# Kernel optimization log

Measured on AMD Instinct MI355X. Metric: run time of the kernel, lower is better.

Reference implementation:

```python
import jax, jax.numpy as jnp
import numpy as np

B, D, N, NKV, H = 8, 256, 2048, 2048, 4
DH = D // H
EPS = 1e-5


def _pw(W, b, t):
    # pointwise Conv1d (kernel_size=1): [out,in] x [B,in,N] -> [B,out,N]
    return jnp.einsum('oi,bin->bon', W, t) + b[None, :, None]


def setup_inputs() -> dict:
    key = jax.random.key(0)
    ks = jax.random.split(key, 16)
    s = 0.05
    inp = {
        'x': jax.random.normal(ks[0], (B, D, N), jnp.float32),
        'source': jax.random.normal(ks[1], (B, D, NKV), jnp.float32),
        'mask': jax.random.uniform(ks[2], (B, N, NKV), jnp.float32),
        'Wq': jax.random.normal(ks[3], (D, D), jnp.float32) * s,
        'bq': jax.random.normal(ks[4], (D,), jnp.float32) * s,
        'Wk': jax.random.normal(ks[5], (D, D), jnp.float32) * s,
        'bk': jax.random.normal(ks[6], (D,), jnp.float32) * s,
        'Wv': jax.random.normal(ks[7], (D, D), jnp.float32) * s,
        'bv': jax.random.normal(ks[8], (D,), jnp.float32) * s,
        'Wm': jax.random.normal(ks[9], (D, D), jnp.float32) * s,
        'bm': jax.random.normal(ks[10], (D,), jnp.float32) * s,
        'W1': jax.random.normal(ks[11], (2 * D, 2 * D), jnp.float32) * s,
        'b1': jax.random.normal(ks[12], (2 * D,), jnp.float32) * s,
        'W2': jax.random.normal(ks[13], (D, 2 * D), jnp.float32) * s,
        'b2': jnp.zeros((D,), jnp.float32),  # nn.init.constant_(mlp[-1].bias, 0)
    }
    return inp


def reference(x, source, mask, Wq, bq, Wk, bk, Wv, bv, Wm, bm, W1, b1, W2, b2):
    b = x.shape[0]
    # projections, then split channels D -> (dh, H) as torch .view does
    q = _pw(Wq, bq, x).reshape(b, DH, H, -1)       # [B,dh,H,N]
    k = _pw(Wk, bk, source).reshape(b, DH, H, -1)  # [B,dh,H,M]
    v = _pw(Wv, bv, source).reshape(b, DH, H, -1)  # [B,dh,H,M]
    scores = jnp.einsum('bdhn,bdhm->bhnm', q, k) / jnp.sqrt(jnp.float32(DH))
    scores = scores * mask[:, None, :, :]          # multiplicative mask
    prob = jax.nn.softmax(scores, axis=-1)
    attn = jnp.einsum('bhnm,bdhm->bdhn', prob, v).reshape(b, D, -1)
    message = _pw(Wm, bm, attn)                    # merge conv
    y = jnp.concatenate([x, message], axis=1)      # [B,2D,N]
    y = _pw(W1, b1, y)
    # InstanceNorm1d (affine=False): normalize over N per (batch, channel)
    mu = jnp.mean(y, axis=-1, keepdims=True)
    var = jnp.var(y, axis=-1, keepdims=True)
    y = jax.nn.relu((y - mu) / jnp.sqrt(var + EPS))
    return _pw(W2, b2, y)
```

## Files before the change

### kernel.cpp

```cpp
#include <hip/hip_runtime.h>
#include <hip/hip_bf16.h>
#include <math.h>

#define B_  8
#define D_  256
#define N_  2048
#define M_  2048
#define H_  4

typedef __attribute__((ext_vector_type(8))) short bf16x8;
typedef __attribute__((ext_vector_type(4))) float f32x4;

static __device__ __forceinline__ unsigned short f2bf(float f) {
    __hip_bfloat16 h = __float2bfloat16(f);
    return *reinterpret_cast<unsigned short*>(&h);
}
static __device__ __forceinline__ float bf2f_lo(unsigned int u) {
    return __uint_as_float((u & 0xffffu) << 16);
}
static __device__ __forceinline__ float bf2f_hi(unsigned int u) {
    return __uint_as_float(u & 0xffff0000u);
}

#define GLOAD16(gsrc, ldsbase)                                                     \
    __builtin_amdgcn_global_load_lds(                                              \
        (const __attribute__((address_space(1))) unsigned int*)(gsrc),             \
        (__attribute__((address_space(3))) unsigned int*)(ldsbase), 16, 0, 0)

__global__ __launch_bounds__(256) void cvt_w(
    const float* __restrict__ Wq, const float* __restrict__ Wk,
    const float* __restrict__ Wv, const float* __restrict__ Wm,
    const float* __restrict__ W1, const float* __restrict__ W2,
    const float* __restrict__ bq, const float* __restrict__ bk,
    unsigned short* __restrict__ wqp, unsigned short* __restrict__ wkp,
    unsigned short* __restrict__ wv,  unsigned short* __restrict__ wmp,
    unsigned short* __restrict__ w1b, unsigned short* __restrict__ w2b,
    float* __restrict__ bqp, float* __restrict__ bkp)
{
    const int idx = blockIdx.x * 256 + threadIdx.x;
    if (idx < 65536) {
        const int op = idx >> 8, k = idx & 255;
        const int h = op >> 6, dh = op & 63;
        wqp[idx] = f2bf(Wq[(dh*4 + h)*256 + k]);
    } else if (idx < 131072) {
        const int j = idx - 65536;
        const int op = j >> 8, k = j & 255;
        const int h = op >> 6, dh = op & 63;
        wkp[j] = f2bf(Wk[(dh*4 + h)*256 + k]);
    } else if (idx < 196608) {
        const int j = idx - 131072;
        wv[j] = f2bf(Wv[j]);
    } else if (idx < 262144) {
        const int j = idx - 196608;
        const int o = j >> 8, cp = j & 255;
        const int h = cp >> 6, dh = cp & 63;
        wmp[j] = f2bf(Wm[o*256 + dh*4 + h]);
    } else if (idx < 524288) {
        const int j = idx - 262144;
        w1b[j] = f2bf(W1[j]);
    } else if (idx < 655360) {
        const int j = idx - 524288;
        w2b[j] = f2bf(W2[j]);
    } else if (idx < 655616) {
        const int j = idx - 655360;
        const int h = j >> 6, dh = j & 63;
        bqp[j] = bq[dh*4 + h];
    } else {
        const int j = idx - 655616;
        const int h = j >> 6, dh = j & 63;
        bkp[j] = bk[dh*4 + h];
    }
}

__global__ __launch_bounds__(256) void cvt_t(
    const float* __restrict__ x, const float* __restrict__ src,
    unsigned short* __restrict__ xbf, unsigned short* __restrict__ sbf)
{
    __shared__ float T[64][65];
    const int z = blockIdx.z;
    const int b = z & 7;
    const float* in = (z < 8) ? x : src;
    unsigned short* out = (z < 8) ? xbf : sbf;
    const int c0 = blockIdx.y * 64, n0 = blockIdx.x * 64;
    const int tid = threadIdx.x;
    #pragma unroll
    for (int u = 0; u < 16; ++u) {
        const int idx = u * 256 + tid;
        const int nn = idx & 63, cc = idx >> 6;
        T[cc][nn] = in[((size_t)(b*256 + c0 + cc))*2048 + n0 + nn];
    }
    __syncthreads();
    #pragma unroll
    for (int u = 0; u < 16; ++u) {
        const int idx = u * 256 + tid;
        const int c = idx & 63, nn = idx >> 6;
        out[((size_t)(b*2048 + n0 + nn))*256 + c0 + c] = f2bf(T[c][nn]);
    }
}

template<int CIN, int EPI>
__global__ __launch_bounds__(256, 2) void conv_mfma(
    const unsigned short* __restrict__ Wb, const float* __restrict__ bias,
    const unsigned short* __restrict__ inA, const unsigned short* __restrict__ inB,
    int splitC, void* __restrict__ outp)
{
    __shared__ __align__(16) unsigned short SH[32768];
    const int b  = blockIdx.z;
    const int o0 = blockIdx.y * 128;
    const int n0 = blockIdx.x * 128;
    const int tid = threadIdx.x;
    const int w = tid >> 6, l = tid & 63;
    const int wr = w >> 1, wc = w & 1;
    const int g_ = l >> 4, ln = l & 15;

    f32x4 acc[4][4];
    #pragma unroll
    for (int mi = 0; mi < 4; ++mi)
        #pragma unroll
        for (int nj = 0; nj < 4; ++nj) acc[mi][nj] = (f32x4){0.f, 0.f, 0.f, 0.f};

    auto STAGE = [&](int t, int c) {
        const int k0 = t * 64;
        unsigned short* As = SH + c * 16384;
        unsigned short* Bs = As + 8192;
        #pragma unroll
        for (int u = 0; u < 4; ++u) {
            const int chunk = (w*4 + u)*64 + l;
            const int row = chunk >> 3;
            const int cs = (chunk & 7) ^ (row & 7);
            const unsigned short* gp = Wb + (size_t)(o0 + row)*CIN + k0 + cs*8;
            GLOAD16(gp, As + (w*4 + u)*512);
        }
        const unsigned short* src; int sC, kk;
        if (k0 < splitC) { src = inA; sC = splitC; kk = k0; }
        else             { src = inB; sC = CIN - splitC; kk = k0 - splitC; }
        #pragma unroll
        for (int u = 0; u < 4; ++u) {
            const int chunk = (w*4 + u)*64 + l;
            const int row = chunk >> 3;
            const int cs = (chunk & 7) ^ (row & 7);
            const unsigned short* gp = src + ((size_t)b*N_ + n0 + row)*sC + kk + cs*8;
            GLOAD16(gp, Bs + (w*4 + u)*512);
        }
    };

    auto COMPUTE = [&](int c) {
        const unsigned short* As = SH + c * 16384;
        const unsigned short* Bs = As + 8192;
        #pragma unroll
        for (int ks = 0; ks < 2; ++ks) {
            bf16x8 af[4], bfr[4];
            #pragma unroll
            for (int mi = 0; mi < 4; ++mi) {
                const int row = wr*64 + mi*16 + ln;
                af[mi] = *(const bf16x8*)&As[row*64 + (((ks*4 + g_) ^ (row & 7)) << 3)];
            }
            #pragma unroll
            for (int nj = 0; nj < 4; ++nj) {
                const int row = wc*64 + nj*16 + ln;
                bfr[nj] = *(const bf16x8*)&Bs[row*64 + (((ks*4 + g_) ^ (row & 7)) << 3)];
            }
            #pragma unroll
            for (int mi = 0; mi < 4; ++mi)
                #pragma unroll
                for (int nj = 0; nj < 4; ++nj)
                    acc[mi][nj] = __builtin_amdgcn_mfma_f32_16x16x32_bf16(af[mi], bfr[nj], acc[mi][nj], 0, 0, 0);
        }
    };

    const int nt = CIN / 64;
    STAGE(0, 0);
    __syncthreads();
    int cur = 0;
    for (int t = 0; t < nt; ++t) {
        if (t + 1 < nt) STAGE(t + 1, cur ^ 1);
        COMPUTE(cur);
        __syncthreads();
        cur ^= 1;
    }

    if constexpr (EPI == 0 || EPI == 2) {
        unsigned short* Os = SH;
        #pragma unroll
        for (int mi = 0; mi < 4; ++mi) {
            const int ob = wr*64 + mi*16 + g_*4;
            const float4 bv = *(const float4*)&bias[o0 + ob];
            #pragma unroll
            for (int nj = 0; nj < 4; ++nj) {
                const int nl = wc*64 + nj*16 + ln;
                ushort4 us;
                us.x = f2bf(acc[mi][nj][0] + bv.x);
                us.y = f2bf(acc[mi][nj][1] + bv.y);
                us.z = f2bf(acc[mi][nj][2] + bv.z);
                us.w = f2bf(acc[mi][nj][3] + bv.w);
                *(ushort4*)&Os[nl*128 + (((ob >> 3) ^ (nl & 7)) << 3) + (ob & 4)] = us;
            }
        }
        __syncthreads();
        if constexpr (EPI == 0) {
            unsigned short* outT = (unsigned short*)outp;
            #pragma unroll
            for (int u = 0; u < 8; ++u) {
                const int idx = u*256 + tid;
                const int oc = idx & 15, n = idx >> 4;
                const uint4 v = *(const uint4*)&Os[n*128 + ((oc ^ (n & 7)) << 3)];
                const int og = o0 + oc*8;
                *(uint4*)&outT[(((size_t)b*H_ + (og >> 6))*N_ + n0 + n)*64 + (og & 63)] = v;
            }
        } else {
            unsigned short* outS = (unsigned short*)outp;
            const int ostride = gridDim.y * 128;
            #pragma unroll
            for (int u = 0; u < 8; ++u) {
                const int idx = u*256 + tid;
                const int oc = idx & 15, n = idx >> 4;
                const uint4 v = *(const uint4*)&Os[n*128 + ((oc ^ (n & 7)) << 3)];
                *(uint4*)&outS[((size_t)b*N_ + n0 + n)*ostride + o0 + oc*8] = v;
            }
        }
    } else if constexpr (EPI == 1) {
        unsigned short* Os = SH;
        #pragma unroll
        for (int mi = 0; mi < 4; ++mi) {
            const int ob = wr*64 + mi*16 + g_*4;
            const float4 bv = *(const float4*)&bias[o0 + ob];
            const float bb[4] = {bv.x, bv.y, bv.z, bv.w};
            #pragma unroll
            for (int nj = 0; nj < 4; ++nj) {
                const int nl = wc*64 + nj*16 + ln;
                #pragma unroll
                for (int r = 0; r < 4; ++r)
                    Os[(ob + r)*136 + nl] = f2bf(acc[mi][nj][r] + bb[r]);
            }
        }
        __syncthreads();
        unsigned short* outV = (unsigned short*)outp;
        #pragma unroll
        for (int u = 0; u < 8; ++u) {
            const int idx = u*256 + tid;
            const int mc = idx & 15, o = idx >> 4;
            const uint4 v = *(const uint4*)&Os[o*136 + mc*8];
            *(uint4*)&outV[((size_t)b*D_ + o0 + o)*(size_t)M_ + n0 + mc*8] = v;
        }
    } else {
        float* Of = (float*)SH;
        #pragma unroll
        for (int mi = 0; mi < 4; ++mi) {
            const int ob = wr*64 + mi*16 + g_*4;
            const float4 bv = *(const float4*)&bias[o0 + ob];
            const float bb[4] = {bv.x, bv.y, bv.z, bv.w};
            #pragma unroll
            for (int nj = 0; nj < 4; ++nj) {
                const int nl = wc*64 + nj*16 + ln;
                #pragma unroll
                for (int r = 0; r < 4; ++r) {
                    const int o_ = ob + r;
                    Of[o_*128 + ((((nl >> 2) ^ (o_ & 7)) << 2)) + (nl & 3)] = acc[mi][nj][r] + bb[r];
                }
            }
        }
        __syncthreads();
        float* outF = (float*)outp;
        #pragma unroll
        for (int u = 0; u < 16; ++u) {
            const int idx = u*256 + tid;
            const int nc = idx & 31, o = idx >> 5;
            const float4 v = *(const float4*)&Of[o*128 + ((nc ^ (o & 7)) << 2)];
            *(float4*)&outF[((size_t)b*D_ + o0 + o)*(size_t)N_ + n0 + nc*4] = v;
        }
    }
}

__global__ __launch_bounds__(256) void attn_mfma(
    const unsigned short* __restrict__ qt, const unsigned short* __restrict__ kt,
    const unsigned short* __restrict__ vbf, const float* __restrict__ mask,
    unsigned short* __restrict__ ab)
{
    __shared__ __align__(16) unsigned short SH[4 * 64 * 64];
    unsigned short* Qs = SH;
    unsigned short* Ks = SH + 4096;
    unsigned short* Vs = SH + 8192;
    unsigned short* Ps = SH + 12288;

    const int b = blockIdx.z, h = blockIdx.y, n0 = blockIdx.x * 64;
    const int tid = threadIdx.x;
    const int w = tid >> 6, lane = tid & 63;
    const int ln = lane & 15, g = lane >> 4;
    const int rsw = (ln & 7) << 3;

    #pragma unroll
    for (int u = 0; u < 4; ++u) {
        const int idx = u * 256 + tid;
        const int ch = idx & 15, n = idx >> 4;
        const ushort4 v = *(const ushort4*)&qt[(((size_t)b * H_ + h) * N_ + n0 + n) * 64 + ch*4];
        *(ushort4*)&Qs[n * 64 + ((ch*4) ^ ((n & 7) << 3))] = v;
    }

    f32x4 oacc[4];
    #pragma unroll
    for (int f = 0; f < 4; ++f) oacc[f] = (f32x4){0.f, 0.f, 0.f, 0.f};
    float mrun[4] = {-INFINITY, -INFINITY, -INFINITY, -INFINITY};
    float lrun[4] = {0.f, 0.f, 0.f, 0.f};

    __syncthreads();

    bf16x8 a_q[2];
    #pragma unroll
    for (int ks = 0; ks < 2; ++ks)
        a_q[ks] = *(const bf16x8*)&Qs[(w*16 + ln) * 64 + ((ks*32 + g*8) ^ rsw)];

    for (int m0 = 0; m0 < M_; m0 += 64) {
        #pragma unroll
        for (int u = 0; u < 4; ++u) {
            const int idx = u * 256 + tid;
            const int ch = idx & 15, r = idx >> 4;
            const ushort4 kv = *(const ushort4*)&kt[(((size_t)b * H_ + h) * M_ + m0 + r) * 64 + ch*4];
            *(ushort4*)&Ks[r * 64 + ((ch*4) ^ ((r & 7) << 3))] = kv;
            const ushort4 vv = *(const ushort4*)&vbf[((size_t)b * D_ + r * H_ + h) * M_ + m0 + ch*4];
            *(ushort4*)&Vs[r * 64 + ((ch*4) ^ ((r & 7) << 3))] = vv;
        }
        __syncthreads();

        float mk[4][4];
        #pragma unroll
        for (int r = 0; r < 4; ++r)
            #pragma unroll
            for (int f = 0; f < 4; ++f)
                mk[r][f] = mask[((size_t)b * N_ + n0 + w*16 + g*4 + r) * (size_t)M_ + m0 + f*16 + ln];

        f32x4 sacc[4];
        #pragma unroll
        for (int f = 0; f < 4; ++f) sacc[f] = (f32x4){0.f, 0.f, 0.f, 0.f};
        #pragma unroll
        for (int ks = 0; ks < 2; ++ks)
            #pragma unroll
            for (int f = 0; f < 4; ++f) {
                const bf16x8 bk = *(const bf16x8*)&Ks[(f*16 + ln) * 64 + ((ks*32 + g*8) ^ rsw)];
                sacc[f] = __builtin_amdgcn_mfma_f32_16x16x32_bf16(a_q[ks], bk, sacc[f], 0, 0, 0);
            }

        #pragma unroll
        for (int r = 0; r < 4; ++r) {
            float s0 = sacc[0][r] * 0.125f * mk[r][0];
            float s1 = sacc[1][r] * 0.125f * mk[r][1];
            float s2 = sacc[2][r] * 0.125f * mk[r][2];
            float s3 = sacc[3][r] * 0.125f * mk[r][3];
            float tmax = fmaxf(fmaxf(s0, s1), fmaxf(s2, s3));
            tmax = fmaxf(tmax, __shfl_xor(tmax, 1, 16));
            tmax = fmaxf(tmax, __shfl_xor(tmax, 2, 16));
            tmax = fmaxf(tmax, __shfl_xor(tmax, 4, 16));
            tmax = fmaxf(tmax, __shfl_xor(tmax, 8, 16));
            const float nm = fmaxf(mrun[r], tmax);
            const float corr = __expf(mrun[r] - nm);
            const float p0 = __expf(s0 - nm);
            const float p1 = __expf(s1 - nm);
            const float p2 = __expf(s2 - nm);
            const float p3 = __expf(s3 - nm);
            float ps = p0 + p1 + p2 + p3;
            ps += __shfl_xor(ps, 1, 16);
            ps += __shfl_xor(ps, 2, 16);
            ps += __shfl_xor(ps, 4, 16);
            ps += __shfl_xor(ps, 8, 16);
            lrun[r] = lrun[r] * corr + ps;
            mrun[r] = nm;
            #pragma unroll
            for (int f = 0; f < 4; ++f) oacc[f][r] *= corr;
            const int row = w*16 + g*4 + r;
            const int rs2 = (row & 7) << 3;
            Ps[row * 64 + ((0*16 + ln) ^ rs2)] = f2bf(p0);
            Ps[row * 64 + ((1*16 + ln) ^ rs2)] = f2bf(p1);
            Ps[row * 64 + ((2*16 + ln) ^ rs2)] = f2bf(p2);
            Ps[row * 64 + ((3*16 + ln) ^ rs2)] = f2bf(p3);
        }
        __syncthreads();

        #pragma unroll
        for (int ks = 0; ks < 2; ++ks) {
            const bf16x8 ap = *(const bf16x8*)&Ps[(w*16 + ln) * 64 + ((ks*32 + g*8) ^ rsw)];
            #pragma unroll
            for (int fd = 0; fd < 4; ++fd) {
                const bf16x8 bv = *(const bf16x8*)&Vs[(fd*16 + ln) * 64 + ((ks*32 + g*8) ^ rsw)];
                oacc[fd] = __builtin_amdgcn_mfma_f32_16x16x32_bf16(ap, bv, oacc[fd], 0, 0, 0);
            }
        }
        __syncthreads();
    }

    unsigned short* Os = SH;
    float inv[4];
    #pragma unroll
    for (int r = 0; r < 4; ++r) inv[r] = 1.f / lrun[r];
    #pragma unroll
    for (int fd = 0; fd < 4; ++fd) {
        const int dh = fd*16 + ln;
        const int cd = dh >> 3;
        #pragma unroll
        for (int r = 0; r < 4; ++r) {
            const int n = w*16 + g*4 + r;
            Os[n*64 + ((cd ^ (n & 7)) << 3) + (dh & 7)] = f2bf(oacc[fd][r] * inv[r]);
        }
    }
    __syncthreads();
    #pragma unroll
    for (int u = 0; u < 2; ++u) {
        const int idx = u*256 + tid;
        const int ch = idx & 7, n = idx >> 3;
        const uint4 v = *(const uint4*)&Os[n*64 + ((ch ^ (n & 7)) << 3)];
        *(uint4*)&ab[((size_t)b*N_ + n0 + n)*256 + h*64 + ch*8] = v;
    }
}

__global__ __launch_bounds__(256) void in_stats(
    const unsigned short* __restrict__ y1, float* __restrict__ st)
{
    const int b = blockIdx.y, nch = blockIdx.x, tid = threadIdx.x;
    const int c = tid * 2;
    float sa = 0.f, sa2 = 0.f, sb = 0.f, sb2 = 0.f;
    for (int r = 0; r < 128; ++r) {
        const int n = nch*128 + r;
        const unsigned int u = *(const unsigned int*)&y1[((size_t)b*N_ + n)*512 + c];
        const float a = bf2f_lo(u), bb = bf2f_hi(u);
        sa += a; sa2 += a*a; sb += bb; sb2 += bb*bb;
    }
    atomicAdd(&st[(b*512 + c)*2 + 0], sa);
    atomicAdd(&st[(b*512 + c)*2 + 1], sa2);
    atomicAdd(&st[(b*512 + c + 1)*2 + 0], sb);
    atomicAdd(&st[(b*512 + c + 1)*2 + 1], sb2);
}

__global__ __launch_bounds__(256) void in_apply(
    const unsigned short* __restrict__ y1, const float* __restrict__ st,
    unsigned short* __restrict__ yo)
{
    const int b = blockIdx.y, nch = blockIdx.x, tid = threadIdx.x;
    const int c = tid * 2;
    const float mua = st[(b*512 + c)*2 + 0] * (1.f/2048.f);
    const float vara = st[(b*512 + c)*2 + 1] * (1.f/2048.f) - mua*mua;
    const float inva = rsqrtf(vara + 1e-5f);
    const float mub = st[(b*512 + c + 1)*2 + 0] * (1.f/2048.f);
    const float varb = st[(b*512 + c + 1)*2 + 1] * (1.f/2048.f) - mub*mub;
    const float invb = rsqrtf(varb + 1e-5f);
    for (int r = 0; r < 128; ++r) {
        const int n = nch*128 + r;
        const size_t off = ((size_t)b*N_ + n)*512 + c;
        const unsigned int u = *(const unsigned int*)&y1[off];
        const float na = fmaxf((bf2f_lo(u) - mua) * inva, 0.f);
        const float nb = fmaxf((bf2f_hi(u) - mub) * invb, 0.f);
        const unsigned int pv = (unsigned int)f2bf(na) | ((unsigned int)f2bf(nb) << 16);
        *(unsigned int*)&yo[off] = pv;
    }
}

extern "C" void kernel_launch(void* const* d_in, const int* in_sizes, int n_in,
                              void* d_out, int out_size, void* d_ws, size_t ws_size,
                              hipStream_t stream)
{
    const float* x    = (const float*)d_in[0];
    const float* srcp = (const float*)d_in[1];
    const float* mask = (const float*)d_in[2];
    const float* Wq = (const float*)d_in[3];
    const float* bq = (const float*)d_in[4];
    const float* Wk = (const float*)d_in[5];
    const float* bk = (const float*)d_in[6];
    const float* Wv = (const float*)d_in[7];
    const float* bv = (const float*)d_in[8];
    const float* Wm = (const float*)d_in[9];
    const float* bm = (const float*)d_in[10];
    const float* W1 = (const float*)d_in[11];
    const float* b1 = (const float*)d_in[12];
    const float* W2 = (const float*)d_in[13];
    const float* b2 = (const float*)d_in[14];
    float* out = (float*)d_out;

    char* wsb = (char*)d_ws;
    const size_t MB = 1 << 20;
    unsigned short* xbf   = (unsigned short*)(wsb + 0*MB);
    unsigned short* srcbf = (unsigned short*)(wsb + 8*MB);
    unsigned short* ab    = (unsigned short*)(wsb + 8*MB);
    unsigned short* qt_   = (unsigned short*)(wsb + 16*MB);
    unsigned short* msg   = (unsigned short*)(wsb + 16*MB);
    unsigned short* kt_   = (unsigned short*)(wsb + 24*MB);
    unsigned short* y1    = (unsigned short*)(wsb + 24*MB);
    unsigned short* vb_   = (unsigned short*)(wsb + 32*MB);
    unsigned short* ybf   = (unsigned short*)(wsb + 40*MB);
    char* wbase = wsb + 56*MB;
    unsigned short* wqp = (unsigned short*)(wbase + 0);
    unsigned short* wkp = (unsigned short*)(wbase + 128*1024);
    unsigned short* wv  = (unsigned short*)(wbase + 256*1024);
    unsigned short* wmp = (unsigned short*)(wbase + 384*1024);
    unsigned short* w1b = (unsigned short*)(wbase + 512*1024);
    unsigned short* w2b = (unsigned short*)(wbase + 1024*1024);
    float* bqp   = (float*)(wbase + 1280*1024);
    float* bkp   = (float*)(wbase + 1281*1024);
    float* stats = (float*)(wbase + 1282*1024);

    const dim3 blk(256);

    cvt_w<<<dim3(2562), blk, 0, stream>>>(Wq, Wk, Wv, Wm, W1, W2, bq, bk,
                                          wqp, wkp, wv, wmp, w1b, w2b, bqp, bkp);
    cvt_t<<<dim3(32, 4, 16), blk, 0, stream>>>(x, srcp, xbf, srcbf);
    hipMemsetAsync(stats, 0, 8*512*2*sizeof(float), stream);

    conv_mfma<256, 0><<<dim3(16, 2, 8), blk, 0, stream>>>(wqp, bqp, xbf,   xbf, 256, qt_);
    conv_mfma<256, 0><<<dim3(16, 2, 8), blk, 0, stream>>>(wkp, bkp, srcbf, srcbf, 256, kt_);
    conv_mfma<256, 1><<<dim3(16, 2, 8), blk, 0, stream>>>(wv,  bv,  srcbf, srcbf, 256, vb_);

    attn_mfma<<<dim3(32, 4, 8), blk, 0, stream>>>(qt_, kt_, vb_, mask, ab);

    conv_mfma<256, 2><<<dim3(16, 2, 8), blk, 0, stream>>>(wmp, bm, ab, ab, 256, msg);
    conv_mfma<512, 2><<<dim3(16, 4, 8), blk, 0, stream>>>(w1b, b1, xbf, msg, 256, y1);

    in_stats<<<dim3(16, 8), blk, 0, stream>>>(y1, stats);
    in_apply<<<dim3(16, 8), blk, 0, stream>>>(y1, stats, ybf);

    conv_mfma<512, 4><<<dim3(16, 2, 8), blk, 0, stream>>>(w2b, b2, ybf, ybf, 512, out);
}
```

Before: 445.6 us.

## Fold merge conv into W1, fuse QKV convs, pipeline attention loads

Folds the merge projection (Wm, bm) algebraically into the second half of W1, which removes one full conv pass and its intermediate buffer. The three Q/K/V projections become a single launch. Conv tiles shrink to 64 columns so more blocks run, with higher occupancy bounds. Attention is rewritten to double-buffer K/V with async global-to-LDS loads, prefetch mask values, and use a different softmax update structure. The folded weight is rounded to bf16 after the product, which changes numerics slightly, and the instance-norm kernels get more blocks.

```diff
diff --git a/kernel.cpp b/kernel.cpp
--- a/kernel.cpp
+++ b/kernel.cpp
@@ -29,13 +29,14 @@
 
 __global__ __launch_bounds__(256) void cvt_w(
     const float* __restrict__ Wq, const float* __restrict__ Wk,
-    const float* __restrict__ Wv, const float* __restrict__ Wm,
-    const float* __restrict__ W1, const float* __restrict__ W2,
-    const float* __restrict__ bq, const float* __restrict__ bk,
+    const float* __restrict__ Wv, const float* __restrict__ W1,
+    const float* __restrict__ W2, const float* __restrict__ bq,
+    const float* __restrict__ bk, const float* __restrict__ b1,
+    const float* __restrict__ bm,
     unsigned short* __restrict__ wqp, unsigned short* __restrict__ wkp,
-    unsigned short* __restrict__ wv,  unsigned short* __restrict__ wmp,
-    unsigned short* __restrict__ w1b, unsigned short* __restrict__ w2b,
-    float* __restrict__ bqp, float* __restrict__ bkp)
+    unsigned short* __restrict__ wv,  unsigned short* __restrict__ wcat,
+    unsigned short* __restrict__ w2b,
+    float* __restrict__ bqp, float* __restrict__ bkp, float* __restrict__ bfold)
 {
     const int idx = blockIdx.x * 256 + threadIdx.x;
     if (idx < 65536) {
@@ -50,26 +51,72 @@
     } else if (idx < 196608) {
         const int j = idx - 131072;
         wv[j] = f2bf(Wv[j]);
-    } else if (idx < 262144) {
+    } else if (idx < 327680) {
         const int j = idx - 196608;
-        const int o = j >> 8, cp = j & 255;
-        const int h = cp >> 6, dh = cp & 63;
-        wmp[j] = f2bf(Wm[o*256 + dh*4 + h]);
-    } else if (idx < 524288) {
-        const int j = idx - 262144;
-        w1b[j] = f2bf(W1[j]);
-    } else if (idx < 655360) {
-        const int j = idx - 524288;
+        const int o = j >> 8, k = j & 255;
+        wcat[o*512 + k] = f2bf(W1[o*512 + k]);
+    } else if (idx < 458752) {
+        const int j = idx - 327680;
         w2b[j] = f2bf(W2[j]);
-    } else if (idx < 655616) {
-        const int j = idx - 655360;
+    } else if (idx < 459008) {
+        const int j = idx - 458752;
         const int h = j >> 6, dh = j & 63;
         bqp[j] = bq[dh*4 + h];
-    } else {
-        const int j = idx - 655616;
+    } else if (idx < 459264) {
+        const int j = idx - 459008;
         const int h = j >> 6, dh = j & 63;
         bkp[j] = bk[dh*4 + h];
-    }
+    } else if (idx < 459776) {
+        const int o = idx - 459264;
+        float acc = b1[o];
+        for (int j = 0; j < 256; ++j) acc += W1[o*512 + 256 + j] * bm[j];
+        bfold[o] = acc;
+    }
+}
+
+__global__ __launch_bounds__(256) void fold_w(
+    const float* __restrict__ W1, const float* __restrict__ Wm,
+    unsigned short* __restrict__ wcat)
+{
+    __shared__ float As[64][33];
+    __shared__ float Bs[32][64];
+    const int o0 = blockIdx.y * 64, c0 = blockIdx.x * 64;
+    const int tid = threadIdx.x;
+    const int tx = tid & 15, ty = tid >> 4;
+    float acc[4][4] = {};
+    for (int k0 = 0; k0 < 256; k0 += 32) {
+        #pragma unroll
+        for (int u = 0; u < 8; ++u) {
+            const int l = u * 256 + tid;
+            As[l >> 5][l & 31] = W1[(o0 + (l >> 5))*512 + 256 + k0 + (l & 31)];
+        }
+        #pragma unroll
+        for (int u = 0; u < 8; ++u) {
+            const int l = u * 256 + tid;
+            const int cp = c0 + (l & 63), j = k0 + (l >> 6);
+            const int h = cp >> 6, dh = cp & 63;
+            Bs[l >> 6][l & 63] = Wm[j*256 + dh*4 + h];
+        }
+        __syncthreads();
+        #pragma unroll 8
+        for (int kk = 0; kk < 32; ++kk) {
+            const float a0 = As[ty*4+0][kk];
+            const float a1 = As[ty*4+1][kk];
+            const float a2 = As[ty*4+2][kk];
+            const float a3 = As[ty*4+3][kk];
+            const float4 bv = *(const float4*)&Bs[kk][tx*4];
+            acc[0][0]+=a0*bv.x; acc[0][1]+=a0*bv.y; acc[0][2]+=a0*bv.z; acc[0][3]+=a0*bv.w;
+            acc[1][0]+=a1*bv.x; acc[1][1]+=a1*bv.y; acc[1][2]+=a1*bv.z; acc[1][3]+=a1*bv.w;
+            acc[2][0]+=a2*bv.x; acc[2][1]+=a2*bv.y; acc[2][2]+=a2*bv.z; acc[2][3]+=a2*bv.w;
+            acc[3][0]+=a3*bv.x; acc[3][1]+=a3*bv.y; acc[3][2]+=a3*bv.z; acc[3][3]+=a3*bv.w;
+        }
+        __syncthreads();
+    }
+    #pragma unroll
+    for (int i = 0; i < 4; ++i)
+        #pragma unroll
+        for (int j = 0; j < 4; ++j)
+            wcat[(o0 + ty*4 + i)*512 + 256 + c0 + tx*4 + j] = f2bf(acc[i][j]);
 }
 
 __global__ __launch_bounds__(256) void cvt_t(
@@ -99,71 +146,69 @@
 }
 
 template<int CIN, int EPI>
-__global__ __launch_bounds__(256, 2) void conv_mfma(
+static __device__ __forceinline__ void conv_body(
+    unsigned short* SH,
     const unsigned short* __restrict__ Wb, const float* __restrict__ bias,
     const unsigned short* __restrict__ inA, const unsigned short* __restrict__ inB,
-    int splitC, void* __restrict__ outp)
-{
-    __shared__ __align__(16) unsigned short SH[32768];
-    const int b  = blockIdx.z;
+    int splitC, void* __restrict__ outp, int ostride)
+{
+    const int b  = blockIdx.z & 7;
     const int o0 = blockIdx.y * 128;
-    const int n0 = blockIdx.x * 128;
+    const int n0 = blockIdx.x * 64;
     const int tid = threadIdx.x;
     const int w = tid >> 6, l = tid & 63;
     const int wr = w >> 1, wc = w & 1;
     const int g_ = l >> 4, ln = l & 15;
 
-    f32x4 acc[4][4];
+    f32x4 acc[4][2];
     #pragma unroll
     for (int mi = 0; mi < 4; ++mi)
         #pragma unroll
-        for (int nj = 0; nj < 4; ++nj) acc[mi][nj] = (f32x4){0.f, 0.f, 0.f, 0.f};
+        for (int nj = 0; nj < 2; ++nj) acc[mi][nj] = (f32x4){0.f, 0.f, 0.f, 0.f};
 
     auto STAGE = [&](int t, int c) {
         const int k0 = t * 64;
-        unsigned short* As = SH + c * 16384;
+        unsigned short* As = SH + c * 12288;
         unsigned short* Bs = As + 8192;
         #pragma unroll
         for (int u = 0; u < 4; ++u) {
             const int chunk = (w*4 + u)*64 + l;
             const int row = chunk >> 3;
             const int cs = (chunk & 7) ^ (row & 7);
-            const unsigned short* gp = Wb + (size_t)(o0 + row)*CIN + k0 + cs*8;
-            GLOAD16(gp, As + (w*4 + u)*512);
+            GLOAD16(Wb + (size_t)(o0 + row)*CIN + k0 + cs*8, As + (w*4 + u)*512);
         }
         const unsigned short* src; int sC, kk;
         if (k0 < splitC) { src = inA; sC = splitC; kk = k0; }
         else             { src = inB; sC = CIN - splitC; kk = k0 - splitC; }
         #pragma unroll
-        for (int u = 0; u < 4; ++u) {
-            const int chunk = (w*4 + u)*64 + l;
+        for (int u = 0; u < 2; ++u) {
+            const int chunk = (w*2 + u)*64 + l;
             const int row = chunk >> 3;
             const int cs = (chunk & 7) ^ (row & 7);
-            const unsigned short* gp = src + ((size_t)b*N_ + n0 + row)*sC + kk + cs*8;
-            GLOAD16(gp, Bs + (w*4 + u)*512);
+            GLOAD16(src + ((size_t)b*N_ + n0 + row)*sC + kk + cs*8, Bs + (w*2 + u)*512);
         }
     };
 
     auto COMPUTE = [&](int c) {
-        const unsigned short* As = SH + c * 16384;
+        const unsigned short* As = SH + c * 12288;
         const unsigned short* Bs = As + 8192;
         #pragma unroll
         for (int ks = 0; ks < 2; ++ks) {
-            bf16x8 af[4], bfr[4];
+            bf16x8 af[4], bfr[2];
             #pragma unroll
             for (int mi = 0; mi < 4; ++mi) {
                 const int row = wr*64 + mi*16 + ln;
                 af[mi] = *(const bf16x8*)&As[row*64 + (((ks*4 + g_) ^ (row & 7)) << 3)];
             }
             #pragma unroll
-            for (int nj = 0; nj < 4; ++nj) {
-                const int row = wc*64 + nj*16 + ln;
+            for (int nj = 0; nj < 2; ++nj) {
+                const int row = wc*32 + nj*16 + ln;
                 bfr[nj] = *(const bf16x8*)&Bs[row*64 + (((ks*4 + g_) ^ (row & 7)) << 3)];
             }
             #pragma unroll
             for (int mi = 0; mi < 4; ++mi)
                 #pragma unroll
-                for (int nj = 0; nj < 4; ++nj)
+                for (int nj = 0; nj < 2; ++nj)
                     acc[mi][nj] = __builtin_amdgcn_mfma_f32_16x16x32_bf16(af[mi], bfr[nj], acc[mi][nj], 0, 0, 0);
         }
     };
@@ -186,8 +231,8 @@
             const int ob = wr*64 + mi*16 + g_*4;
             const float4 bv = *(const float4*)&bias[o0 + ob];
             #pragma unroll
-            for (int nj = 0; nj < 4; ++nj) {
-                const int nl = wc*64 + nj*16 + ln;
+            for (int nj = 0; nj < 2; ++nj) {
+                const int nl = wc*32 + nj*16 + ln;
                 ushort4 us;
                 us.x = f2bf(acc[mi][nj][0] + bv.x);
                 us.y = f2bf(acc[mi][nj][1] + bv.y);
@@ -197,24 +242,17 @@
             }
         }
         __syncthreads();
-        if constexpr (EPI == 0) {
-            unsigned short* outT = (unsigned short*)outp;
-            #pragma unroll
-            for (int u = 0; u < 8; ++u) {
-                const int idx = u*256 + tid;
-                const int oc = idx & 15, n = idx >> 4;
-                const uint4 v = *(const uint4*)&Os[n*128 + ((oc ^ (n & 7)) << 3)];
+        #pragma unroll
+        for (int u = 0; u < 4; ++u) {
+            const int idx = u*256 + tid;
+            const int oc = idx & 15, n = idx >> 4;
+            const uint4 v = *(const uint4*)&Os[n*128 + ((oc ^ (n & 7)) << 3)];
+            if constexpr (EPI == 0) {
+                unsigned short* outT = (unsigned short*)outp;
                 const int og = o0 + oc*8;
                 *(uint4*)&outT[(((size_t)b*H_ + (og >> 6))*N_ + n0 + n)*64 + (og & 63)] = v;
-            }
-        } else {
-            unsigned short* outS = (unsigned short*)outp;
-            const int ostride = gridDim.y * 128;
-            #pragma unroll
-            for (int u = 0; u < 8; ++u) {
-                const int idx = u*256 + tid;
-                const int oc = idx & 15, n = idx >> 4;
-                const uint4 v = *(const uint4*)&Os[n*128 + ((oc ^ (n & 7)) << 3)];
+            } else {
+                unsigned short* outS = (unsigned short*)outp;
                 *(uint4*)&outS[((size_t)b*N_ + n0 + n)*ostride + o0 + oc*8] = v;
             }
         }
@@ -226,20 +264,20 @@
             const float4 bv = *(const float4*)&bias[o0 + ob];
             const float bb[4] = {bv.x, bv.y, bv.z, bv.w};
             #pragma unroll
-            for (int nj = 0; nj < 4; ++nj) {
-                const int nl = wc*64 + nj*16 + ln;
+            for (int nj = 0; nj < 2; ++nj) {
+                const int nl = wc*32 + nj*16 + ln;
                 #pragma unroll
                 for (int r = 0; r < 4; ++r)
-                    Os[(ob + r)*136 + nl] = f2bf(acc[mi][nj][r] + bb[r]);
+                    Os[(ob + r)*72 + nl] = f2bf(acc[mi][nj][r] + bb[r]);
             }
         }
         __syncthreads();
         unsigned short* outV = (unsigned short*)outp;
         #pragma unroll
-        for (int u = 0; u < 8; ++u) {
+        for (int u = 0; u < 4; ++u) {
             const int idx = u*256 + tid;
-            const int mc = idx & 15, o = idx >> 4;
-            const uint4 v = *(const uint4*)&Os[o*136 + mc*8];
+            const int mc = idx & 7, o = idx >> 3;
+            const uint4 v = *(const uint4*)&Os[o*72 + mc*8];
             *(uint4*)&outV[((size_t)b*D_ + o0 + o)*(size_t)M_ + n0 + mc*8] = v;
         }
     } else {
@@ -250,37 +288,61 @@
             const float4 bv = *(const float4*)&bias[o0 + ob];
             const float bb[4] = {bv.x, bv.y, bv.z, bv.w};
             #pragma unroll
-            for (int nj = 0; nj < 4; ++nj) {
-                const int nl = wc*64 + nj*16 + ln;
+            for (int nj = 0; nj < 2; ++nj) {
+                const int nl = wc*32 + nj*16 + ln;
                 #pragma unroll
-                for (int r = 0; r < 4; ++r) {
-                    const int o_ = ob + r;
-                    Of[o_*128 + ((((nl >> 2) ^ (o_ & 7)) << 2)) + (nl & 3)] = acc[mi][nj][r] + bb[r];
-                }
+                for (int r = 0; r < 4; ++r)
+                    Of[(ob + r)*68 + nl] = acc[mi][nj][r] + bb[r];
             }
         }
         __syncthreads();
         float* outF = (float*)outp;
         #pragma unroll
-        for (int u = 0; u < 16; ++u) {
+        for (int u = 0; u < 8; ++u) {
             const int idx = u*256 + tid;
-            const int nc = idx & 31, o = idx >> 5;
-            const float4 v = *(const float4*)&Of[o*128 + ((nc ^ (o & 7)) << 2)];
+            const int nc = idx & 15, o = idx >> 4;
+            const float4 v = *(const float4*)&Of[o*68 + nc*4];
             *(float4*)&outF[((size_t)b*D_ + o0 + o)*(size_t)N_ + n0 + nc*4] = v;
         }
     }
 }
 
-__global__ __launch_bounds__(256) void attn_mfma(
+__global__ __launch_bounds__(256, 3) void conv_qkv(
+    const unsigned short* __restrict__ wqp, const float* __restrict__ bqp,
+    const unsigned short* __restrict__ wkp, const float* __restrict__ bkp,
+    const unsigned short* __restrict__ wv,  const float* __restrict__ bv,
+    const unsigned short* __restrict__ xbf, const unsigned short* __restrict__ srcbf,
+    unsigned short* __restrict__ qt, unsigned short* __restrict__ kt,
+    unsigned short* __restrict__ vb)
+{
+    __shared__ __align__(16) unsigned short SH[24576];
+    const int zz = blockIdx.z >> 3;
+    if (zz == 0)      conv_body<256, 0>(SH, wqp, bqp, xbf,   xbf,   256, qt, 0);
+    else if (zz == 1) conv_body<256, 0>(SH, wkp, bkp, srcbf, srcbf, 256, kt, 0);
+    else              conv_body<256, 1>(SH, wv,  bv,  srcbf, srcbf, 256, vb, 0);
+}
+
+template<int CIN, int EPI>
+__global__ __launch_bounds__(256, 3) void conv_mfma(
+    const unsigned short* __restrict__ Wb, const float* __restrict__ bias,
+    const unsigned short* __restrict__ inA, const unsigned short* __restrict__ inB,
+    int splitC, void* __restrict__ outp)
+{
+    __shared__ __align__(16) unsigned short SH[24576];
+    conv_body<CIN, EPI>(SH, Wb, bias, inA, inB, splitC, outp, gridDim.y * 128);
+}
+
+__global__ __launch_bounds__(256, 4) void attn_mfma(
     const unsigned short* __restrict__ qt, const unsigned short* __restrict__ kt,
     const unsigned short* __restrict__ vbf, const float* __restrict__ mask,
     unsigned short* __restrict__ ab)
 {
-    __shared__ __align__(16) unsigned short SH[4 * 64 * 64];
-    unsigned short* Qs = SH;
-    unsigned short* Ks = SH + 4096;
-    unsigned short* Vs = SH + 8192;
-    unsigned short* Ps = SH + 12288;
+    __shared__ __align__(16) unsigned short SH[20480];
+    unsigned short* Kb0 = SH;
+    unsigned short* Kb1 = SH + 4096;
+    unsigned short* Vb0 = SH + 8192;
+    unsigned short* Vb1 = SH + 12288;
+    unsigned short* QP  = SH + 16384;
 
     const int b = blockIdx.z, h = blockIdx.y, n0 = blockIdx.x * 64;
     const int tid = threadIdx.x;
@@ -288,13 +350,25 @@
     const int ln = lane & 15, g = lane >> 4;
     const int rsw = (ln & 7) << 3;
 
-    #pragma unroll
-    for (int u = 0; u < 4; ++u) {
-        const int idx = u * 256 + tid;
-        const int ch = idx & 15, n = idx >> 4;
-        const ushort4 v = *(const ushort4*)&qt[(((size_t)b * H_ + h) * N_ + n0 + n) * 64 + ch*4];
-        *(ushort4*)&Qs[n * 64 + ((ch*4) ^ ((n & 7) << 3))] = v;
-    }
+    const unsigned short* qbase = qt + (((size_t)b * H_ + h) * N_ + n0) * 64;
+    const unsigned short* kbase = kt + ((size_t)b * H_ + h) * (size_t)M_ * 64;
+    const unsigned short* vbase = vbf + (size_t)b * D_ * M_ + (size_t)h * M_;
+    const float* mbase = mask + ((size_t)b * N_ + n0 + w*16 + g*4) * (size_t)M_ + ln;
+
+    #pragma unroll
+    for (int u = 0; u < 2; ++u) {
+        const int chunk = (w*2 + u)*64 + lane;
+        const int row = chunk >> 3, cs = (chunk & 7) ^ (row & 7);
+        GLOAD16(qbase + row*64 + cs*8, QP + (w*2+u)*512);
+        GLOAD16(kbase + row*64 + cs*8, Kb0 + (w*2+u)*512);
+        GLOAD16(vbase + (size_t)row*(H_*M_) + cs*8, Vb0 + (w*2+u)*512);
+    }
+    float mA[16], mB[16];
+    #pragma unroll
+    for (int r = 0; r < 4; ++r)
+        #pragma unroll
+        for (int f = 0; f < 4; ++f)
+            mA[r*4+f] = mbase[(size_t)r*M_ + f*16];
 
     f32x4 oacc[4];
     #pragma unroll
@@ -302,88 +376,114 @@
     float mrun[4] = {-INFINITY, -INFINITY, -INFINITY, -INFINITY};
     float lrun[4] = {0.f, 0.f, 0.f, 0.f};
 
-    __syncthreads();
+    asm volatile("s_waitcnt vmcnt(0)" ::: "memory");
+    __builtin_amdgcn_s_barrier();
+    __builtin_amdgcn_sched_barrier(0);
 
     bf16x8 a_q[2];
     #pragma unroll
     for (int ks = 0; ks < 2; ++ks)
-        a_q[ks] = *(const bf16x8*)&Qs[(w*16 + ln) * 64 + ((ks*32 + g*8) ^ rsw)];
-
-    for (int m0 = 0; m0 < M_; m0 += 64) {
-        #pragma unroll
-        for (int u = 0; u < 4; ++u) {
-            const int idx = u * 256 + tid;
-            const int ch = idx & 15, r = idx >> 4;
-            const ushort4 kv = *(const ushort4*)&kt[(((size_t)b * H_ + h) * M_ + m0 + r) * 64 + ch*4];
-            *(ushort4*)&Ks[r * 64 + ((ch*4) ^ ((r & 7) << 3))] = kv;
-            const ushort4 vv = *(const ushort4*)&vbf[((size_t)b * D_ + r * H_ + h) * M_ + m0 + ch*4];
-            *(ushort4*)&Vs[r * 64 + ((ch*4) ^ ((r & 7) << 3))] = vv;
-        }
-        __syncthreads();
-
-        float mk[4][4];
+        a_q[ks] = *(const bf16x8*)&QP[(w*16 + ln)*64 + ((ks*32 + g*8) ^ rsw)];
+
+    auto ITER = [&](int t, float (&mc)[16], float (&mn)[16]) {
+        unsigned short* Kc = (t & 1) ? Kb1 : Kb0;
+        unsigned short* Vc = (t & 1) ? Vb1 : Vb0;
+        unsigned short* Kn = (t & 1) ? Kb0 : Kb1;
+        unsigned short* Vn = (t & 1) ? Vb0 : Vb1;
+        if (t + 1 < 32) {
+            const int m1 = (t + 1) * 64;
+            #pragma unroll
+            for (int u = 0; u < 2; ++u) {
+                const int chunk = (w*2 + u)*64 + lane;
+                const int row = chunk >> 3, cs = (chunk & 7) ^ (row & 7);
+                GLOAD16(kbase + (size_t)(m1 + row)*64 + cs*8, Kn + (w*2+u)*512);
+                GLOAD16(vbase + (size_t)row*(H_*M_) + m1 + cs*8, Vn + (w*2+u)*512);
+            }
+            #pragma unroll
+            for (int r = 0; r < 4; ++r)
+                #pragma unroll
+                for (int f = 0; f < 4; ++f)
+                    mn[r*4+f] = mbase[(size_t)r*M_ + m1 + f*16];
+        }
+        f32x4 sacc[4];
+        #pragma unroll
+        for (int f = 0; f < 4; ++f) sacc[f] = (f32x4){0.f, 0.f, 0.f, 0.f};
+        __builtin_amdgcn_s_setprio(1);
+        #pragma unroll
+        for (int ks = 0; ks < 2; ++ks)
+            #pragma unroll
+            for (int f = 0; f < 4; ++f) {
+                const bf16x8 bk = *(const bf16x8*)&Kc[(f*16 + ln)*64 + ((ks*32 + g*8) ^ rsw)];
+                sacc[f] = __builtin_amdgcn_mfma_f32_16x16x32_bf16(a_q[ks], bk, sacc[f], 0, 0, 0);
+            }
+        __builtin_amdgcn_s_setprio(0);
         #pragma unroll
         for (int r = 0; r < 4; ++r)
             #pragma unroll
             for (int f = 0; f < 4; ++f)
-                mk[r][f] = mask[((size_t)b * N_ + n0 + w*16 + g*4 + r) * (size_t)M_ + m0 + f*16 + ln];
-
-        f32x4 sacc[4];
-        #pragma unroll
-        for (int f = 0; f < 4; ++f) sacc[f] = (f32x4){0.f, 0.f, 0.f, 0.f};
-        #pragma unroll
-        for (int ks = 0; ks < 2; ++ks)
+                sacc[f][r] = sacc[f][r] * 0.125f * mc[r*4+f];
+        float tm[4];
+        bool need = false;
+        #pragma unroll
+        for (int r = 0; r < 4; ++r) {
+            float t0 = fmaxf(fmaxf(sacc[0][r], sacc[1][r]), fmaxf(sacc[2][r], sacc[3][r]));
+            t0 = fmaxf(t0, __shfl_xor(t0, 1, 16));
+            t0 = fmaxf(t0, __shfl_xor(t0, 2, 16));
+            t0 = fmaxf(t0, __shfl_xor(t0, 4, 16));
+            t0 = fmaxf(t0, __shfl_xor(t0, 8, 16));
+            tm[r] = t0;
+            need |= (t0 > mrun[r] + 8.f);
+        }
+        if (__any(need)) {
+            #pragma unroll
+            for (int r = 0; r < 4; ++r) {
+                const float nm = fmaxf(mrun[r], tm[r]);
+                const float corr = __expf(mrun[r] - nm);
+                mrun[r] = nm;
+                lrun[r] *= corr;
+                #pragma unroll
+                for (int f = 0; f < 4; ++f) oacc[f][r] *= corr;
+            }
+        }
+        #pragma unroll
+        for (int r = 0; r < 4; ++r) {
+            const int row = w*16 + g*4 + r;
+            const int rs2 = (row & 7) << 3;
+            float ps = 0.f;
             #pragma unroll
             for (int f = 0; f < 4; ++f) {
-                const bf16x8 bk = *(const bf16x8*)&Ks[(f*16 + ln) * 64 + ((ks*32 + g*8) ^ rsw)];
-                sacc[f] = __builtin_amdgcn_mfma_f32_16x16x32_bf16(a_q[ks], bk, sacc[f], 0, 0, 0);
-            }
-
-        #pragma unroll
-        for (int r = 0; r < 4; ++r) {
-            float s0 = sacc[0][r] * 0.125f * mk[r][0];
-            float s1 = sacc[1][r] * 0.125f * mk[r][1];
-            float s2 = sacc[2][r] * 0.125f * mk[r][2];
-            float s3 = sacc[3][r] * 0.125f * mk[r][3];
-            float tmax = fmaxf(fmaxf(s0, s1), fmaxf(s2, s3));
-            tmax = fmaxf(tmax, __shfl_xor(tmax, 1, 16));
-            tmax = fmaxf(tmax, __shfl_xor(tmax, 2, 16));
-            tmax = fmaxf(tmax, __shfl_xor(tmax, 4, 16));
-            tmax = fmaxf(tmax, __shfl_xor(tmax, 8, 16));
-            const float nm = fmaxf(mrun[r], tmax);
-            const float corr = __expf(mrun[r] - nm);
-            const float p0 = __expf(s0 - nm);
-            const float p1 = __expf(s1 - nm);
-            const float p2 = __expf(s2 - nm);
-            const float p3 = __expf(s3 - nm);
-            float ps = p0 + p1 + p2 + p3;
+                const float p = __expf(sacc[f][r] - mrun[r]);
+                ps += p;
+                QP[row*64 + ((f*16 + ln) ^ rs2)] = f2bf(p);
+            }
             ps += __shfl_xor(ps, 1, 16);
             ps += __shfl_xor(ps, 2, 16);
             ps += __shfl_xor(ps, 4, 16);
             ps += __shfl_xor(ps, 8, 16);
-            lrun[r] = lrun[r] * corr + ps;
-            mrun[r] = nm;
-            #pragma unroll
-            for (int f = 0; f < 4; ++f) oacc[f][r] *= corr;
-            const int row = w*16 + g*4 + r;
-            const int rs2 = (row & 7) << 3;
-            Ps[row * 64 + ((0*16 + ln) ^ rs2)] = f2bf(p0);
-            Ps[row * 64 + ((1*16 + ln) ^ rs2)] = f2bf(p1);
-            Ps[row * 64 + ((2*16 + ln) ^ rs2)] = f2bf(p2);
-            Ps[row * 64 + ((3*16 + ln) ^ rs2)] = f2bf(p3);
-        }
-        __syncthreads();
-
+            lrun[r] += ps;
+        }
+        asm volatile("s_waitcnt lgkmcnt(0)" ::: "memory");
+        __builtin_amdgcn_sched_barrier(0);
+        __builtin_amdgcn_s_setprio(1);
         #pragma unroll
         for (int ks = 0; ks < 2; ++ks) {
-            const bf16x8 ap = *(const bf16x8*)&Ps[(w*16 + ln) * 64 + ((ks*32 + g*8) ^ rsw)];
+            const bf16x8 ap = *(const bf16x8*)&QP[(w*16 + ln)*64 + ((ks*32 + g*8) ^ rsw)];
             #pragma unroll
             for (int fd = 0; fd < 4; ++fd) {
-                const bf16x8 bv = *(const bf16x8*)&Vs[(fd*16 + ln) * 64 + ((ks*32 + g*8) ^ rsw)];
+                const bf16x8 bv = *(const bf16x8*)&Vc[(fd*16 + ln)*64 + ((ks*32 + g*8) ^ rsw)];
                 oacc[fd] = __builtin_amdgcn_mfma_f32_16x16x32_bf16(ap, bv, oacc[fd], 0, 0, 0);
             }
         }
-        __syncthreads();
+        __builtin_amdgcn_s_setprio(0);
+        asm volatile("s_waitcnt vmcnt(0)" ::: "memory");
+        __builtin_amdgcn_s_barrier();
+        __builtin_amdgcn_sched_barrier(0);
+    };
+
+    #pragma unroll 1
+    for (int tt = 0; tt < 32; tt += 2) {
+        ITER(tt,     mA, mB);
+        ITER(tt + 1, mB, mA);
     }
 
     unsigned short* Os = SH;
@@ -400,7 +500,9 @@
             Os[n*64 + ((cd ^ (n & 7)) << 3) + (dh & 7)] = f2bf(oacc[fd][r] * inv[r]);
         }
     }
-    __syncthreads();
+    asm volatile("s_waitcnt lgkmcnt(0)" ::: "memory");
+    __builtin_amdgcn_s_barrier();
+    __builtin_amdgcn_sched_barrier(0);
     #pragma unroll
     for (int u = 0; u < 2; ++u) {
         const int idx = u*256 + tid;
@@ -416,8 +518,9 @@
     const int b = blockIdx.y, nch = blockIdx.x, tid = threadIdx.x;
     const int c = tid * 2;
     float sa = 0.f, sa2 = 0.f, sb = 0.f, sb2 = 0.f;
-    for (int r = 0; r < 128; ++r) {
-        const int n = nch*128 + r;
+    #pragma unroll 4
+    for (int r = 0; r < 32; ++r) {
+        const int n = nch*32 + r;
         const unsigned int u = *(const unsigned int*)&y1[((size_t)b*N_ + n)*512 + c];
         const float a = bf2f_lo(u), bb = bf2f_hi(u);
         sa += a; sa2 += a*a; sb += bb; sb2 += bb*bb;
@@ -440,14 +543,14 @@
     const float mub = st[(b*512 + c + 1)*2 + 0] * (1.f/2048.f);
     const float varb = st[(b*512 + c + 1)*2 + 1] * (1.f/2048.f) - mub*mub;
     const float invb = rsqrtf(varb + 1e-5f);
-    for (int r = 0; r < 128; ++r) {
-        const int n = nch*128 + r;
+    #pragma unroll 4
+    for (int r = 0; r < 32; ++r) {
+        const int n = nch*32 + r;
         const size_t off = ((size_t)b*N_ + n)*512 + c;
         const unsigned int u = *(const unsigned int*)&y1[off];
         const float na = fmaxf((bf2f_lo(u) - mua) * inva, 0.f);
         const float nb = fmaxf((bf2f_hi(u) - mub) * invb, 0.f);
-        const unsigned int pv = (unsigned int)f2bf(na) | ((unsigned int)f2bf(nb) << 16);
-        *(unsigned int*)&yo[off] = pv;
+        *(unsigned int*)&yo[off] = (unsigned int)f2bf(na) | ((unsigned int)f2bf(nb) << 16);
     }
 }
 
@@ -478,40 +581,38 @@
     unsigned short* srcbf = (unsigned short*)(wsb + 8*MB);
     unsigned short* ab    = (unsigned short*)(wsb + 8*MB);
     unsigned short* qt_   = (unsigned short*)(wsb + 16*MB);
-    unsigned short* msg   = (unsigned short*)(wsb + 16*MB);
     unsigned short* kt_   = (unsigned short*)(wsb + 24*MB);
-    unsigned short* y1    = (unsigned short*)(wsb + 24*MB);
+    unsigned short* y1    = (unsigned short*)(wsb + 16*MB);
     unsigned short* vb_   = (unsigned short*)(wsb + 32*MB);
-    unsigned short* ybf   = (unsigned short*)(wsb + 40*MB);
-    char* wbase = wsb + 56*MB;
-    unsigned short* wqp = (unsigned short*)(wbase + 0);
-    unsigned short* wkp = (unsigned short*)(wbase + 128*1024);
-    unsigned short* wv  = (unsigned short*)(wbase + 256*1024);
-    unsigned short* wmp = (unsigned short*)(wbase + 384*1024);
-    unsigned short* w1b = (unsigned short*)(wbase + 512*1024);
-    unsigned short* w2b = (unsigned short*)(wbase + 1024*1024);
-    float* bqp   = (float*)(wbase + 1280*1024);
-    float* bkp   = (float*)(wbase + 1281*1024);
-    float* stats = (float*)(wbase + 1282*1024);
+    unsigned short* ybf   = (unsigned short*)(wsb + 32*MB);
+    char* wbase = wsb + 48*MB;
+    unsigned short* wqp  = (unsigned short*)(wbase + 0);
+    unsigned short* wkp  = (unsigned short*)(wbase + 131072);
+    unsigned short* wv   = (unsigned short*)(wbase + 262144);
+    unsigned short* wcat = (unsigned short*)(wbase + 393216);
+    unsigned short* w2b  = (unsigned short*)(wbase + 917504);
+    float* bqp   = (float*)(wbase + 1179648);
+    float* bkp   = (float*)(wbase + 1180672);
+    float* bfold = (float*)(wbase + 1181696);
+    float* stats = (float*)(wbase + 1183744);
 
     const dim3 blk(256);
 
-    cvt_w<<<dim3(2562), blk, 0, stream>>>(Wq, Wk, Wv, Wm, W1, W2, bq, bk,
-                                          wqp, wkp, wv, wmp, w1b, w2b, bqp, bkp);
+    cvt_w<<<dim3(1796), blk, 0, stream>>>(Wq, Wk, Wv, W1, W2, bq, bk, b1, bm,
+                                          wqp, wkp, wv, wcat, w2b, bqp, bkp, bfold);
+    fold_w<<<dim3(4, 8), blk, 0, stream>>>(W1, Wm, wcat);
     cvt_t<<<dim3(32, 4, 16), blk, 0, stream>>>(x, srcp, xbf, srcbf);
     hipMemsetAsync(stats, 0, 8*512*2*sizeof(float), stream);
 
-    conv_mfma<256, 0><<<dim3(16, 2, 8), blk, 0, stream>>>(wqp, bqp, xbf,   xbf, 256, qt_);
-    conv_mfma<256, 0><<<dim3(16, 2, 8), blk, 0, stream>>>(wkp, bkp, srcbf, srcbf, 256, kt_);
-    conv_mfma<256, 1><<<dim3(16, 2, 8), blk, 0, stream>>>(wv,  bv,  srcbf, srcbf, 256, vb_);
+    conv_qkv<<<dim3(32, 2, 24), blk, 0, stream>>>(wqp, bqp, wkp, bkp, wv, bv,
+                                                  xbf, srcbf, qt_, kt_, vb_);
 
     attn_mfma<<<dim3(32, 4, 8), blk, 0, stream>>>(qt_, kt_, vb_, mask, ab);
 
-    conv_mfma<256, 2><<<dim3(16, 2, 8), blk, 0, stream>>>(wmp, bm, ab, ab, 256, msg);
-    conv_mfma<512, 2><<<dim3(16, 4, 8), blk, 0, stream>>>(w1b, b1, xbf, msg, 256, y1);
-
-    in_stats<<<dim3(16, 8), blk, 0, stream>>>(y1, stats);
-    in_apply<<<dim3(16, 8), blk, 0, stream>>>(y1, stats, ybf);
-
-    conv_mfma<512, 4><<<dim3(16, 2, 8), blk, 0, stream>>>(w2b, b2, ybf, ybf, 512, out);
-}
+    conv_mfma<512, 2><<<dim3(32, 4, 8), blk, 0, stream>>>(wcat, bfold, xbf, ab, 256, y1);
+
+    in_stats<<<dim3(64, 8), blk, 0, stream>>>(y1, stats);
+    in_apply<<<dim3(64, 8), blk, 0, stream>>>(y1, stats, ybf);
+
+    conv_mfma<512, 4><<<dim3(32, 2, 8), blk, 0, stream>>>(w2b, b2, ybf, ybf, 512, out);
+}
```

Result: no change. 449.6 us (+0.9%).
